# Kernel tuning notes

Hardware: AMD Instinct MI355X
Metric: run time of the kernel (lower is better)

Reference implementation:

```python
import jax, jax.numpy as jnp
import numpy as np
import math

D = 1024
H = 16
FF = 4096
BS = 4
N = 1024
NEG_INF = -jnp.inf


def layer_norm(x, g, b, eps=1e-5):
    mu = jnp.mean(x, axis=-1, keepdims=True)
    var = jnp.var(x, axis=-1, keepdims=True)
    return (x - mu) * jax.lax.rsqrt(var + eps) * g + b


def mha(x, kv, Wq, Wk, Wv, g, b, causal):
    bs, n, d = x.shape
    n_kv = kv.shape[1]
    hd = d // H
    q = (x @ Wq).reshape(bs, n, H, hd)
    k = (kv @ Wk).reshape(bs, n_kv, H, hd)
    v = (kv @ Wv).reshape(bs, n_kv, H, hd)
    # scores scaled by 1/sqrt(model_dim) as in the original (not head_dim!)
    scores = jnp.einsum('bihd,bjhd->bhij', q, k) / math.sqrt(d)
    if causal:
        i = jnp.arange(n)[:, None]
        j = jnp.arange(n_kv)[None, :]
        scores = jnp.where(j <= i, scores, NEG_INF)
    probs = jax.nn.softmax(scores, axis=-1)
    ctx = jnp.einsum('bhij,bjhd->bihd', probs, v).reshape(bs, n, d)
    return layer_norm(ctx + x, g, b)


def setup_inputs() -> dict:
    key = jax.random.key(0)
    ks = jax.random.split(key, 20)
    s_attn = 1.0 / math.sqrt(D)
    s_ff1 = 1.0 / math.sqrt(D)
    s_ff2 = 1.0 / math.sqrt(FF)
    return {
        'x': jax.random.normal(ks[0], (BS, N, D), jnp.float32),
        'encoder_out': jax.random.normal(ks[1], (BS, N, D), jnp.float32),
        'Wq1': jax.random.normal(ks[2], (D, D), jnp.float32) * s_attn,
        'Wk1': jax.random.normal(ks[3], (D, D), jnp.float32) * s_attn,
        'Wv1': jax.random.normal(ks[4], (D, D), jnp.float32) * s_attn,
        'g1': jnp.ones((D,), jnp.float32), 'b1': jnp.zeros((D,), jnp.float32),
        'Wq2': jax.random.normal(ks[5], (D, D), jnp.float32) * s_attn,
        'Wk2': jax.random.normal(ks[6], (D, D), jnp.float32) * s_attn,
        'Wv2': jax.random.normal(ks[7], (D, D), jnp.float32) * s_attn,
        'g2': jnp.ones((D,), jnp.float32), 'b2': jnp.zeros((D,), jnp.float32),
        'W_ff1': jax.random.normal(ks[8], (D, FF), jnp.float32) * s_ff1,
        'b_ff1': jnp.zeros((FF,), jnp.float32),
        'W_ff2': jax.random.normal(ks[9], (FF, D), jnp.float32) * s_ff2,
        'b_ff2': jnp.zeros((D,), jnp.float32),
        'g3': jnp.ones((D,), jnp.float32), 'b3': jnp.zeros((D,), jnp.float32),
    }


def reference(x, encoder_out, Wq1, Wk1, Wv1, g1, b1, Wq2, Wk2, Wv2, g2, b2,
              W_ff1, b_ff1, W_ff2, b_ff2, g3, b3):
    # masked (causal) self-attention
    x = mha(x, x, Wq1, Wk1, Wv1, g1, b1, causal=True)
    # cross-attention over encoder output
    x = mha(x, encoder_out, Wq2, Wk2, Wv2, g2, b2, causal=False)
    # feedforward with exact GELU, residual, layernorm
    h = jax.nn.gelu(x @ W_ff1 + b_ff1, approximate=False)
    out = h @ W_ff2 + b_ff2
    return layer_norm(out + x, g3, b3)
```

## Files before the change

### kernel.cpp

```cpp
#include <hip/hip_runtime.h>

typedef unsigned short u16;
typedef short bf16x8 __attribute__((ext_vector_type(8)));
typedef float f32x4 __attribute__((ext_vector_type(4)));
typedef unsigned short u16x8 __attribute__((ext_vector_type(8)));
typedef unsigned short u16x4 __attribute__((ext_vector_type(4)));

__device__ __forceinline__ u16 f2bf(float f) {
  unsigned u = __builtin_bit_cast(unsigned, f);
  u += 0x7fffu + ((u >> 16) & 1u);
  return (u16)(u >> 16);
}
__device__ __forceinline__ float bf2f(u16 v) {
  return __builtin_bit_cast(float, (unsigned)v << 16);
}

__device__ __forceinline__ void gload_lds16(const void* g, void* l) {
  __builtin_amdgcn_global_load_lds(
      (const __attribute__((address_space(1))) unsigned int*)g,
      (__attribute__((address_space(3))) unsigned int*)l, 16, 0, 0);
}

__global__ __launch_bounds__(256) void cast2_bf16_kernel(const float* __restrict__ s0,
                                                         u16* __restrict__ d0,
                                                         const float* __restrict__ s1,
                                                         u16* __restrict__ d1) {
  const float* s = blockIdx.y ? s1 : s0;
  u16* d = blockIdx.y ? d1 : d0;
  const size_t i = (size_t)blockIdx.x * 256 + threadIdx.x;
  const float4 a = ((const float4*)s)[2 * i];
  const float4 b = ((const float4*)s)[2 * i + 1];
  u16x8 o;
  o[0] = f2bf(a.x); o[1] = f2bf(a.y); o[2] = f2bf(a.z); o[3] = f2bf(a.w);
  o[4] = f2bf(b.x); o[5] = f2bf(b.y); o[6] = f2bf(b.z); o[7] = f2bf(b.w);
  ((u16x8*)d)[i] = o;
}

__global__ __launch_bounds__(256) void pack_mega_kernel(
    const float* __restrict__ W0, const float* __restrict__ W1,
    const float* __restrict__ W2, const float* __restrict__ W3,
    const float* __restrict__ W4, const float* __restrict__ W5,
    const float* __restrict__ W6, const float* __restrict__ W7,
    u16* __restrict__ out) {
  const int bid = blockIdx.x;
  const float* W;
  int K, N, local;
  size_t dst0;
  if (bid < 1536) {
    const int w = bid >> 8;
    local = bid & 255;
    K = 1024; N = 1024;
    W = (w == 0) ? W0 : (w == 1) ? W1 : (w == 2) ? W2 : (w == 3) ? W3 : (w == 4) ? W4 : W5;
    dst0 = (size_t)w * 1024 * 1024;
  } else if (bid < 2560) {
    local = bid - 1536;
    K = 1024; N = 4096; W = W6;
    dst0 = (size_t)6 * 1024 * 1024;
  } else {
    local = bid - 2560;
    K = 4096; N = 1024; W = W7;
    dst0 = (size_t)10 * 1024 * 1024;
  }
  const int nx = N >> 6;
  const int n0 = (local % nx) << 6, k0 = (local / nx) << 6;
  __shared__ u16 sh[64][72];
  const int t = threadIdx.x;
  {
    const int kloc = t >> 2, nc = (t & 3) * 16;
    const float* src = W + (size_t)(k0 + kloc) * N + n0 + nc;
#pragma unroll
    for (int i = 0; i < 16; ++i) sh[kloc][nc + i] = f2bf(src[i]);
  }
  __syncthreads();
  {
    const int nloc = t >> 2, kc = (t & 3) * 16;
    u16 tmp[16];
#pragma unroll
    for (int i = 0; i < 16; ++i) tmp[i] = sh[kc + i][nloc];
    u16* dst = out + dst0 + (size_t)(n0 + nloc) * K + k0 + kc;
    *(u16x8*)dst = *(const u16x8*)tmp;
    *(u16x8*)(dst + 8) = *(const u16x8*)(tmp + 8);
  }
}

template <int EPI, int VOUT>
__global__ __launch_bounds__(512, 4) void gemm_bt(const u16* __restrict__ A,
                                                  const u16* __restrict__ Bt,
                                                  void* __restrict__ Cout,
                                                  const float* __restrict__ bias,
                                                  u16* __restrict__ vt, int voff,
                                                  int M, int N, int K, int lda, int ldb) {
  __shared__ u16 lds[2][2][128 * 64];
  const int tid = threadIdx.x;
  const int lane = tid & 63;
  const int wid = tid >> 6;
  const int wr = wid >> 2;
  const int wc = wid & 3;
  const int g = lane >> 4, cc = lane & 15;
  const int nb = N >> 7;
  const int nwg = gridDim.x;
  const int cpx = nwg >> 3;
  const int bid = (blockIdx.x & 7) * cpx + (blockIdx.x >> 3);
  const int bm = bid / nb, bn = bid % nb;
  const size_t arow0 = (size_t)bm << 7;
  const size_t brow0 = (size_t)bn << 7;
  const size_t koff = (size_t)blockIdx.y * K;

  const u16* ap[2];
  const u16* bp[2];
  int ldst[2];
#pragma unroll
  for (int i = 0; i < 2; ++i) {
    const int tt = i * 512 + tid;
    const int row = tt >> 3;
    const int sc8 = ((tt & 7) ^ (row & 7)) * 8;
    ap[i] = A + (arow0 + row) * lda + koff + sc8;
    bp[i] = Bt + (brow0 + row) * ldb + koff + sc8;
    ldst[i] = (i * 512 + wid * 64) * 8;
  }

  int aoff[4], boff[2];
#pragma unroll
  for (int m = 0; m < 4; ++m) {
    const int rowa = wr * 64 + m * 16 + cc;
    aoff[m] = rowa * 128 + ((g ^ (rowa & 7)) << 4);
  }
#pragma unroll
  for (int n = 0; n < 2; ++n) {
    const int rowb = wc * 32 + n * 16 + cc;
    boff[n] = rowb * 128 + ((g ^ (rowb & 7)) << 4);
  }

  f32x4 acc[4][2] = {};
  const int nk = K >> 6;

#pragma unroll
  for (int i = 0; i < 2; ++i) {
    gload_lds16(ap[i], &lds[0][0][ldst[i]]);
    gload_lds16(bp[i], &lds[0][1][ldst[i]]);
    ap[i] += 64;
    bp[i] += 64;
  }
  __syncthreads();

  int cur = 0;
  for (int kk = 0; kk < nk; ++kk) {
    if (kk + 1 < nk) {
#pragma unroll
      for (int i = 0; i < 2; ++i) {
        gload_lds16(ap[i], &lds[cur ^ 1][0][ldst[i]]);
        gload_lds16(bp[i], &lds[cur ^ 1][1][ldst[i]]);
        ap[i] += 64;
        bp[i] += 64;
      }
    }
    const char* Al = (const char*)&lds[cur][0][0];
    const char* Bl = (const char*)&lds[cur][1][0];
    __builtin_amdgcn_s_setprio(1);
#pragma unroll
    for (int ks = 0; ks < 2; ++ks) {
      const int xr = ks << 6;
      bf16x8 af[4], bfr[2];
#pragma unroll
      for (int m = 0; m < 4; ++m)
        af[m] = *(const bf16x8*)(Al + (aoff[m] ^ xr));
#pragma unroll
      for (int n = 0; n < 2; ++n)
        bfr[n] = *(const bf16x8*)(Bl + (boff[n] ^ xr));
#pragma unroll
      for (int m = 0; m < 4; ++m)
#pragma unroll
        for (int n = 0; n < 2; ++n)
          acc[m][n] = __builtin_amdgcn_mfma_f32_16x16x32_bf16(af[m], bfr[n],
                                                              acc[m][n], 0, 0, 0);
    }
    __builtin_amdgcn_s_setprio(0);
    __syncthreads();
    cur ^= 1;
  }

  const size_t pout = (size_t)blockIdx.y * M * N;
#pragma unroll
  for (int m = 0; m < 4; ++m) {
    const size_t gr0 = arow0 + wr * 64 + m * 16 + (g << 2);
#pragma unroll
    for (int n = 0; n < 2; ++n) {
      const size_t gc = brow0 + wc * 32 + n * 16 + cc;
      if (VOUT && (int)gc >= voff) {
        const int col = (int)gc - voff;
        const int hh = col >> 6, dd = col & 63;
        const int bb = (int)(gr0 >> 10), nn = (int)(gr0 & 1023);
        u16x4 ov;
#pragma unroll
        for (int r = 0; r < 4; ++r) ov[r] = f2bf(acc[m][n][r]);
        *(u16x4*)&vt[(((size_t)(bb * 16 + hh) * 64 + dd) << 10) + nn] = ov;
        continue;
      }
      float bv = 0.f;
      if constexpr (EPI == 1) bv = bias[gc];
#pragma unroll
      for (int r = 0; r < 4; ++r) {
        float v = acc[m][n][r] + bv;
        const size_t idx = (gr0 + r) * (size_t)N + gc;
        if constexpr (EPI == 1) {
          const float u2 = 1.5957691216f * (v + 0.044715f * v * v * v);
          const float e = __expf(u2);
          v = v * e / (e + 1.f);
          ((u16*)Cout)[idx] = f2bf(v);
        } else if constexpr (EPI == 0) {
          ((u16*)Cout)[idx] = f2bf(v);
        } else {
          ((u16*)Cout)[pout + idx] = f2bf(v);
        }
      }
    }
  }
}

template <int CAUSAL, int NZ>
__global__ __launch_bounds__(256, 6) void attn_kernel(const u16* __restrict__ Qb,
                                                      const u16* __restrict__ Kb,
                                                      const u16* __restrict__ Vt,
                                                      u16* __restrict__ Opart,
                                                      float* __restrict__ lpart,
                                                      int qstride, int kstride) {
  const int qt = blockIdx.x;
  const int bh = blockIdx.y;
  const int z = (NZ == 2) ? blockIdx.z : 0;
  const int b = bh >> 4, h = bh & 15;
  const int lane = threadIdx.x & 63;
  const int w = threadIdx.x >> 6;
  const int g = lane >> 4, c = lane & 15;
  const int qbase = qt * 64 + w * 16;

  u16* Op = Opart + (size_t)z * 4096 * 1024;
  float* lp = (NZ == 2) ? lpart + (size_t)z * 64 * 1024 + (size_t)bh * 1024 : nullptr;

  int kt0 = z * (16 / NZ), kt1 = kt0 + 16 / NZ;
  if (CAUSAL) kt1 = min(kt1, qt + 1);

  if (NZ == 2 && kt1 <= kt0) {
#pragma unroll
    for (int r = 0; r < 4; ++r) {
      const int qrow = qbase + g * 4 + r;
      u16x4 zz = {0, 0, 0, 0};
      *(u16x4*)&Op[(size_t)(b * 1024 + qrow) * 1024 + h * 64 + c * 4] = zz;
      if (c == 0) lp[qrow] = 0.f;
    }
    return;
  }

  bf16x8 qf0, qf1;
  {
    const int qrow = qbase + c;
    const u16* qp = Qb + (size_t)(b * 1024 + qrow) * qstride + h * 64 + g * 8;
    qf0 = *(const bf16x8*)qp;
    qf1 = *(const bf16x8*)(qp + 32);
  }

  float l_part[4] = {0.f, 0.f, 0.f, 0.f};
  f32x4 oacc[4] = {};

  __shared__ u16 Kl[64 * 64];
  __shared__ u16 Vl[64 * 64];
  __shared__ u16 Pl[4][16 * 72];
  u16* pw = &Pl[w][0];
  const int tid = threadIdx.x;

  for (int kt = kt0; kt < kt1; ++kt) {
    const int kv0 = kt * 64;
    __syncthreads();
#pragma unroll
    for (int i = 0; i < 2; ++i) {
      const int tt = i * 256 + tid;
      const int row = tt >> 3;
      const int sc = (tt & 7) ^ (row & 7);
      gload_lds16(Kb + (size_t)(b * 1024 + kv0 + row) * kstride + h * 64 + sc * 8,
                  &Kl[(size_t)(i * 256 + w * 64) * 8]);
      gload_lds16(Vt + ((size_t)bh * 64 + row) * 1024 + kv0 + sc * 8,
                  &Vl[(size_t)(i * 256 + w * 64) * 8]);
    }
    __syncthreads();

    f32x4 sacc[4] = {};
#pragma unroll
    for (int t = 0; t < 4; ++t) {
      const int row = t * 16 + c;
      const bf16x8 kf0 = *(const bf16x8*)&Kl[row * 64 + (g ^ (row & 7)) * 8];
      const bf16x8 kf1 = *(const bf16x8*)&Kl[row * 64 + ((4 + g) ^ (row & 7)) * 8];
      sacc[t] = __builtin_amdgcn_mfma_f32_16x16x32_bf16(qf0, kf0, sacc[t], 0, 0, 0);
      sacc[t] = __builtin_amdgcn_mfma_f32_16x16x32_bf16(qf1, kf1, sacc[t], 0, 0, 0);
    }
    const int qr0 = qbase + g * 4;
#pragma unroll
    for (int t = 0; t < 4; ++t) {
      const int kvcol = kv0 + t * 16 + c;
      const int col = t * 16 + c;
#pragma unroll
      for (int r = 0; r < 4; ++r) {
        float p = __expf(sacc[t][r] * 0.03125f);
        if (CAUSAL && kvcol > qr0 + r) p = 0.f;
        l_part[r] += p;
        pw[(g * 4 + r) * 72 + col] = f2bf(p);
      }
    }
#pragma unroll
    for (int ks = 0; ks < 2; ++ks) {
      const bf16x8 pa = *(const bf16x8*)&pw[c * 72 + ks * 32 + g * 8];
#pragma unroll
      for (int t2 = 0; t2 < 4; ++t2) {
        const int row = t2 * 16 + c;
        const bf16x8 vb =
            *(const bf16x8*)&Vl[row * 64 + ((ks * 4 + g) ^ (row & 7)) * 8];
        oacc[t2] = __builtin_amdgcn_mfma_f32_16x16x32_bf16(pa, vb, oacc[t2], 0, 0, 0);
      }
    }
  }
#pragma unroll
  for (int xm = 1; xm < 16; xm <<= 1)
#pragma unroll
    for (int r = 0; r < 4; ++r) l_part[r] += __shfl_xor(l_part[r], xm);

  if constexpr (NZ == 2) {
    if (c == 0) {
#pragma unroll
      for (int r = 0; r < 4; ++r) lp[qbase + g * 4 + r] = l_part[r];
    }
#pragma unroll
    for (int t2 = 0; t2 < 4; ++t2) {
      const int d = t2 * 16 + c;
#pragma unroll
      for (int r = 0; r < 4; ++r) {
        const int qrow = qbase + g * 4 + r;
        Op[(size_t)(b * 1024 + qrow) * 1024 + h * 64 + d] = f2bf(oacc[t2][r]);
      }
    }
  } else {
    float rl[4];
#pragma unroll
    for (int r = 0; r < 4; ++r) rl[r] = 1.f / l_part[r];
#pragma unroll
    for (int t2 = 0; t2 < 4; ++t2) {
      const int d = t2 * 16 + c;
#pragma unroll
      for (int r = 0; r < 4; ++r) {
        const int qrow = qbase + g * 4 + r;
        Op[(size_t)(b * 1024 + qrow) * 1024 + h * 64 + d] = f2bf(oacc[t2][r] * rl[r]);
      }
    }
  }
}

template <int MODE, int RES_BF, int OUT_F>
__global__ __launch_bounds__(256) void add_ln_kernel(const void* __restrict__ a,
                                                     const float* __restrict__ lpart,
                                                     const void* __restrict__ res,
                                                     const float* __restrict__ gam,
                                                     const float* __restrict__ bet,
                                                     float* __restrict__ yf,
                                                     u16* __restrict__ ybf,
                                                     const float* __restrict__ bias) {
  const size_t row = blockIdx.x;
  const int t = threadIdx.x;
  float x[4];
  if constexpr (MODE == 1) {
    const u16* Ob = (const u16*)a;
    const u16x4 p0 = ((const u16x4*)(Ob + row * 1024))[t];
    const u16x4 p1 = ((const u16x4*)(Ob + (size_t)4096 * 1024 + row * 1024))[t];
    const int b = (int)(row >> 10), q = (int)(row & 1023);
    const int h = t >> 4;
    const size_t li = (size_t)(b * 16 + h) * 1024 + q;
    const float inv = 1.f / (lpart[li] + lpart[(size_t)64 * 1024 + li]);
#pragma unroll
    for (int i = 0; i < 4; ++i) x[i] = (bf2f(p0[i]) + bf2f(p1[i])) * inv;
  } else if constexpr (MODE == 2) {
    const u16* Ob = (const u16*)a;
    const u16x4 p0 = ((const u16x4*)(Ob + row * 1024))[t];
    const u16x4 p1 = ((const u16x4*)(Ob + (size_t)4096 * 1024 + row * 1024))[t];
    const float4 bv2 = ((const float4*)bias)[t];
    x[0] = bf2f(p0[0]) + bf2f(p1[0]) + bv2.x;
    x[1] = bf2f(p0[1]) + bf2f(p1[1]) + bv2.y;
    x[2] = bf2f(p0[2]) + bf2f(p1[2]) + bv2.z;
    x[3] = bf2f(p0[3]) + bf2f(p1[3]) + bv2.w;
  } else {
    const u16* Ob = (const u16*)a;
    const u16x4 p0 = ((const u16x4*)(Ob + row * 1024))[t];
#pragma unroll
    for (int i = 0; i < 4; ++i) x[i] = bf2f(p0[i]);
  }
  if constexpr (RES_BF) {
    const u16x4 rv = ((const u16x4*)((const u16*)res + row * 1024))[t];
#pragma unroll
    for (int i = 0; i < 4; ++i) x[i] += bf2f(rv[i]);
  } else {
    const float4 rv = ((const float4*)((const float*)res + row * 1024))[t];
    x[0] += rv.x; x[1] += rv.y; x[2] += rv.z; x[3] += rv.w;
  }
  float s = x[0] + x[1] + x[2] + x[3];
  float q2 = x[0] * x[0] + x[1] * x[1] + x[2] * x[2] + x[3] * x[3];
#pragma unroll
  for (int m = 1; m < 64; m <<= 1) { s += __shfl_xor(s, m); q2 += __shfl_xor(q2, m); }
  __shared__ float ss[4], sq[4];
  const int w = t >> 6;
  if ((t & 63) == 0) { ss[w] = s; sq[w] = q2; }
  __syncthreads();
  s = ss[0] + ss[1] + ss[2] + ss[3];
  q2 = sq[0] + sq[1] + sq[2] + sq[3];
  const float mu = s * (1.f / 1024.f);
  const float var = q2 * (1.f / 1024.f) - mu * mu;
  const float rstd = rsqrtf(var + 1e-5f);
  const float4 gv = ((const float4*)gam)[t];
  const float4 bv = ((const float4*)bet)[t];
  float y[4];
  y[0] = (x[0] - mu) * rstd * gv.x + bv.x;
  y[1] = (x[1] - mu) * rstd * gv.y + bv.y;
  y[2] = (x[2] - mu) * rstd * gv.z + bv.z;
  y[3] = (x[3] - mu) * rstd * gv.w + bv.w;
  if constexpr (OUT_F) {
    float4 o; o.x = y[0]; o.y = y[1]; o.z = y[2]; o.w = y[3];
    ((float4*)(yf + row * 1024))[t] = o;
  } else {
    u16x4 ob;
    ob[0] = f2bf(y[0]); ob[1] = f2bf(y[1]); ob[2] = f2bf(y[2]); ob[3] = f2bf(y[3]);
    ((u16x4*)(ybf + row * 1024))[t] = ob;
  }
}

extern "C" void kernel_launch(void* const* d_in, const int* in_sizes, int n_in,
                              void* d_out, int out_size, void* d_ws, size_t ws_size,
                              hipStream_t stream) {
  const float* x    = (const float*)d_in[0];
  const float* enc  = (const float*)d_in[1];
  const float* Wq1  = (const float*)d_in[2];
  const float* Wk1  = (const float*)d_in[3];
  const float* Wv1  = (const float*)d_in[4];
  const float* g1   = (const float*)d_in[5];
  const float* b1   = (const float*)d_in[6];
  const float* Wq2  = (const float*)d_in[7];
  const float* Wk2  = (const float*)d_in[8];
  const float* Wv2  = (const float*)d_in[9];
  const float* g2   = (const float*)d_in[10];
  const float* b2   = (const float*)d_in[11];
  const float* Wff1 = (const float*)d_in[12];
  const float* bff1 = (const float*)d_in[13];
  const float* Wff2 = (const float*)d_in[14];
  const float* bff2 = (const float*)d_in[15];
  const float* g3   = (const float*)d_in[16];
  const float* b3   = (const float*)d_in[17];
  float* out = (float*)d_out;

  char* ws = (char*)d_ws;
  const size_t MB = 1024ull * 1024ull;
  const size_t M1 = 1024ull * 1024ull;
  u16*   big   = (u16*)(ws + 8 * MB);
  u16*   vt    = (u16*)(ws + 40 * MB);
  u16*   opart = (u16*)(ws + 48 * MB);
  u16*   wpack = (u16*)(ws + 64 * MB);
  float* lpart = (float*)(ws + 92 * MB);
  u16*   abf   = (u16*)(ws + 96 * MB);
  u16*   ebf   = (u16*)(ws + 104 * MB);
  (void)in_sizes; (void)n_in; (void)out_size; (void)ws_size;

  cast2_bf16_kernel<<<dim3(2048, 2), 256, 0, stream>>>(x, abf, enc, ebf);
  pack_mega_kernel<<<3584, 256, 0, stream>>>(Wq1, Wk1, Wv1, Wq2, Wk2, Wv2,
                                             Wff1, Wff2, wpack);

  gemm_bt<0, 1><<<(4096 / 128) * (3072 / 128), 512, 0, stream>>>(
      abf, wpack, big, nullptr, vt, 2048, 4096, 3072, 1024, 1024, 1024);
  attn_kernel<1, 2><<<dim3(16, 64, 2), 256, 0, stream>>>(big, big + 1024, vt,
                                                         opart, lpart, 3072, 3072);
  add_ln_kernel<1, 0, 0><<<4096, 256, 0, stream>>>(opart, lpart, x, g1, b1,
                                                   nullptr, abf, nullptr);

  u16* q2  = big;
  u16* kv2 = big + (size_t)4096 * 1024;
  gemm_bt<0, 0><<<(4096 / 128) * (1024 / 128), 512, 0, stream>>>(
      abf, wpack + 3 * M1, q2, nullptr, nullptr, 0, 4096, 1024, 1024, 1024, 1024);
  gemm_bt<0, 1><<<(4096 / 128) * (2048 / 128), 512, 0, stream>>>(
      ebf, wpack + 4 * M1, kv2, nullptr, vt, 1024, 4096, 2048, 1024, 1024, 1024);
  attn_kernel<0, 1><<<dim3(16, 64, 1), 256, 0, stream>>>(q2, kv2, vt,
                                                         opart, nullptr, 1024, 2048);
  add_ln_kernel<3, 1, 0><<<4096, 256, 0, stream>>>(opart, nullptr, abf, g2, b2,
                                                   nullptr, abf, nullptr);

  gemm_bt<1, 0><<<(4096 / 128) * (4096 / 128), 512, 0, stream>>>(
      abf, wpack + 6 * M1, big, bff1, nullptr, 0, 4096, 4096, 1024, 1024, 1024);
  gemm_bt<3, 0><<<dim3((4096 / 128) * (1024 / 128), 2), 512, 0, stream>>>(
      big, wpack + 10 * M1, opart, nullptr, nullptr, 0, 4096, 1024, 2048, 4096, 4096);
  add_ln_kernel<2, 1, 1><<<4096, 256, 0, stream>>>(opart, nullptr, abf, g3, b3,
                                                   out, nullptr, bff2);
}
```

Before: 269.3 us.

## Add 256x256-tile 8-wave GEMM with 4-way split-K for large projections

Introduces gemm8p, a 256x256 output tile GEMM in which each of 8 waves computes 128x64 and the K loop is split into four quarter phases. Each phase interleaves global-to-LDS prefetch of the next tile with MFMA on the current one. It replaces gemm_bt for the QKV, cross-attention KV and FF1 GEMMs, and for FF2, which now uses a 4-way split-K whose partials go to vt and a spare workspace region and are summed in add_ln. The larger tiles raise arithmetic intensity, at the cost of lower occupancy, fewer workgroups (a wave-quantisation risk), and extra partial-sum traffic.

```diff
diff --git a/kernel.cpp b/kernel.cpp
--- a/kernel.cpp
+++ b/kernel.cpp
@@ -84,6 +84,150 @@
 }
 
 template <int EPI, int VOUT>
+__global__ __launch_bounds__(512, 2) void gemm8p(const u16* __restrict__ A,
+                                                 const u16* __restrict__ Bt,
+                                                 void* __restrict__ Cout,
+                                                 const float* __restrict__ bias,
+                                                 u16* __restrict__ vt, int voff,
+                                                 u16* __restrict__ p3,
+                                                 int M, int N, int K, int lda, int ldb) {
+  __shared__ u16 lds[2][4][128 * 64];
+  const int tid = threadIdx.x;
+  const int lane = tid & 63, wid = tid >> 6;
+  const int wr = wid >> 2, wc = wid & 3;
+  const int g = lane >> 4, cc = lane & 15;
+  const int nb = N >> 8;
+  const int nwg = gridDim.x, cpx = nwg >> 3;
+  const int bid = (blockIdx.x & 7) * cpx + (blockIdx.x >> 3);
+  const int bm = bid / nb, bn = bid % nb;
+  const size_t arow0 = (size_t)bm << 8, brow0 = (size_t)bn << 8;
+  const size_t koff = (size_t)blockIdx.y * K;
+
+  const u16* sp[4][2];
+  int dstu[2];
+#pragma unroll
+  for (int j = 0; j < 2; ++j) {
+    const int p = j * 512 + tid;
+    const int rowh = p >> 3;
+    const int sch = (p & 7) ^ (rowh & 7);
+    sp[0][j] = A + (arow0 + rowh) * lda + koff + sch * 8;
+    sp[1][j] = A + (arow0 + 128 + rowh) * lda + koff + sch * 8;
+    sp[2][j] = Bt + (brow0 + rowh) * ldb + koff + sch * 8;
+    sp[3][j] = Bt + (brow0 + 128 + rowh) * ldb + koff + sch * 8;
+    dstu[j] = (j * 512 + wid * 64) * 8;
+  }
+
+  int aoff[8], boff[4];
+#pragma unroll
+  for (int m = 0; m < 8; ++m) {
+    const int r = m * 16 + cc;
+    aoff[m] = r * 128 + ((g ^ (r & 7)) << 4);
+  }
+#pragma unroll
+  for (int n = 0; n < 4; ++n) {
+    const int r = (wc & 1) * 64 + n * 16 + cc;
+    boff[n] = r * 128 + ((g ^ (r & 7)) << 4);
+  }
+  const int bunit = 2 + (wc >> 1);
+
+  f32x4 acc[8][4] = {};
+  const int nt = K >> 6;
+
+#pragma unroll
+  for (int u = 0; u < 4; ++u)
+#pragma unroll
+    for (int j = 0; j < 2; ++j) {
+      gload_lds16(sp[u][j], &lds[0][u][dstu[j]]);
+      sp[u][j] += 64;
+    }
+
+  for (int t = 0; t < nt; ++t) {
+    asm volatile("s_waitcnt vmcnt(0)" ::: "memory");
+    __builtin_amdgcn_s_barrier();
+    __builtin_amdgcn_sched_barrier(0);
+    const int d = t & 1;
+    const char* Au = (const char*)&lds[d][wr][0];
+    const char* Bu = (const char*)&lds[d][bunit][0];
+    const bool pf = (t + 1 < nt);
+#pragma unroll
+    for (int q = 0; q < 4; ++q) {
+      const int qm = q >> 1, qn = q & 1;
+      bf16x8 af[4][2], bf[2][2];
+#pragma unroll
+      for (int m = 0; m < 4; ++m)
+#pragma unroll
+        for (int ks = 0; ks < 2; ++ks)
+          af[m][ks] = *(const bf16x8*)(Au + (aoff[qm * 4 + m] ^ (ks << 6)));
+#pragma unroll
+      for (int n = 0; n < 2; ++n)
+#pragma unroll
+        for (int ks = 0; ks < 2; ++ks)
+          bf[n][ks] = *(const bf16x8*)(Bu + (boff[qn * 2 + n] ^ (ks << 6)));
+      if (pf) {
+#pragma unroll
+        for (int j = 0; j < 2; ++j) {
+          gload_lds16(sp[q][j], &lds[d ^ 1][q][dstu[j]]);
+          sp[q][j] += 64;
+        }
+      }
+      __builtin_amdgcn_s_barrier();
+      asm volatile("s_waitcnt lgkmcnt(0)" ::: "memory");
+      __builtin_amdgcn_sched_barrier(0);
+      __builtin_amdgcn_s_setprio(1);
+#pragma unroll
+      for (int m = 0; m < 4; ++m)
+#pragma unroll
+        for (int n = 0; n < 2; ++n)
+#pragma unroll
+          for (int ks = 0; ks < 2; ++ks)
+            acc[qm * 4 + m][qn * 2 + n] = __builtin_amdgcn_mfma_f32_16x16x32_bf16(
+                af[m][ks], bf[n][ks], acc[qm * 4 + m][qn * 2 + n], 0, 0, 0);
+      __builtin_amdgcn_s_setprio(0);
+      __builtin_amdgcn_s_barrier();
+    }
+  }
+
+  u16* pdst = nullptr;
+  if constexpr (EPI == 3)
+    pdst = (blockIdx.y < 3) ? (u16*)Cout + (size_t)blockIdx.y * M * N : p3;
+#pragma unroll
+  for (int m = 0; m < 8; ++m) {
+    const size_t gr0 = arow0 + wr * 128 + m * 16 + (g << 2);
+#pragma unroll
+    for (int n = 0; n < 4; ++n) {
+      const size_t gc = brow0 + wc * 64 + n * 16 + cc;
+      if (VOUT && (int)gc >= voff) {
+        const int col = (int)gc - voff;
+        const int hh = col >> 6, dd = col & 63;
+        const int bb = (int)(gr0 >> 10), nn = (int)(gr0 & 1023);
+        u16x4 ov;
+#pragma unroll
+        for (int r = 0; r < 4; ++r) ov[r] = f2bf(acc[m][n][r]);
+        *(u16x4*)&vt[(((size_t)(bb * 16 + hh) * 64 + dd) << 10) + nn] = ov;
+        continue;
+      }
+      float bv = 0.f;
+      if constexpr (EPI == 1) bv = bias[gc];
+#pragma unroll
+      for (int r = 0; r < 4; ++r) {
+        float v = acc[m][n][r] + bv;
+        const size_t idx = (gr0 + r) * (size_t)N + gc;
+        if constexpr (EPI == 1) {
+          const float u2 = 1.5957691216f * (v + 0.044715f * v * v * v);
+          const float e = __expf(u2);
+          v = v * e / (e + 1.f);
+          ((u16*)Cout)[idx] = f2bf(v);
+        } else if constexpr (EPI == 0) {
+          ((u16*)Cout)[idx] = f2bf(v);
+        } else {
+          pdst[idx] = f2bf(v);
+        }
+      }
+    }
+  }
+}
+
+template <int EPI, int VOUT>
 __global__ __launch_bounds__(512, 4) void gemm_bt(const u16* __restrict__ A,
                                                   const u16* __restrict__ Bt,
                                                   void* __restrict__ Cout,
@@ -179,7 +323,6 @@
     cur ^= 1;
   }
 
-  const size_t pout = (size_t)blockIdx.y * M * N;
 #pragma unroll
   for (int m = 0; m < 4; ++m) {
     const size_t gr0 = arow0 + wr * 64 + m * 16 + (g << 2);
@@ -209,8 +352,6 @@
           ((u16*)Cout)[idx] = f2bf(v);
         } else if constexpr (EPI == 0) {
           ((u16*)Cout)[idx] = f2bf(v);
-        } else {
-          ((u16*)Cout)[pout + idx] = f2bf(v);
         }
       }
     }
@@ -375,13 +516,16 @@
     for (int i = 0; i < 4; ++i) x[i] = (bf2f(p0[i]) + bf2f(p1[i])) * inv;
   } else if constexpr (MODE == 2) {
     const u16* Ob = (const u16*)a;
+    const u16* P3 = (const u16*)lpart;
     const u16x4 p0 = ((const u16x4*)(Ob + row * 1024))[t];
     const u16x4 p1 = ((const u16x4*)(Ob + (size_t)4096 * 1024 + row * 1024))[t];
+    const u16x4 p2 = ((const u16x4*)(Ob + (size_t)8192 * 1024 + row * 1024))[t];
+    const u16x4 p3 = ((const u16x4*)(P3 + row * 1024))[t];
     const float4 bv2 = ((const float4*)bias)[t];
-    x[0] = bf2f(p0[0]) + bf2f(p1[0]) + bv2.x;
-    x[1] = bf2f(p0[1]) + bf2f(p1[1]) + bv2.y;
-    x[2] = bf2f(p0[2]) + bf2f(p1[2]) + bv2.z;
-    x[3] = bf2f(p0[3]) + bf2f(p1[3]) + bv2.w;
+    x[0] = bf2f(p0[0]) + bf2f(p1[0]) + bf2f(p2[0]) + bf2f(p3[0]) + bv2.x;
+    x[1] = bf2f(p0[1]) + bf2f(p1[1]) + bf2f(p2[1]) + bf2f(p3[1]) + bv2.y;
+    x[2] = bf2f(p0[2]) + bf2f(p1[2]) + bf2f(p2[2]) + bf2f(p3[2]) + bv2.z;
+    x[3] = bf2f(p0[3]) + bf2f(p1[3]) + bf2f(p2[3]) + bf2f(p3[3]) + bv2.w;
   } else {
     const u16* Ob = (const u16*)a;
     const u16x4 p0 = ((const u16x4*)(Ob + row * 1024))[t];
@@ -452,6 +596,7 @@
   char* ws = (char*)d_ws;
   const size_t MB = 1024ull * 1024ull;
   const size_t M1 = 1024ull * 1024ull;
+  u16*   pextra = (u16*)(ws + 0 * MB);
   u16*   big   = (u16*)(ws + 8 * MB);
   u16*   vt    = (u16*)(ws + 40 * MB);
   u16*   opart = (u16*)(ws + 48 * MB);
@@ -459,14 +604,15 @@
   float* lpart = (float*)(ws + 92 * MB);
   u16*   abf   = (u16*)(ws + 96 * MB);
   u16*   ebf   = (u16*)(ws + 104 * MB);
+  u16*   ffpart = vt;
   (void)in_sizes; (void)n_in; (void)out_size; (void)ws_size;
 
   cast2_bf16_kernel<<<dim3(2048, 2), 256, 0, stream>>>(x, abf, enc, ebf);
   pack_mega_kernel<<<3584, 256, 0, stream>>>(Wq1, Wk1, Wv1, Wq2, Wk2, Wv2,
                                              Wff1, Wff2, wpack);
 
-  gemm_bt<0, 1><<<(4096 / 128) * (3072 / 128), 512, 0, stream>>>(
-      abf, wpack, big, nullptr, vt, 2048, 4096, 3072, 1024, 1024, 1024);
+  gemm8p<0, 1><<<(4096 / 256) * (3072 / 256), 512, 0, stream>>>(
+      abf, wpack, big, nullptr, vt, 2048, nullptr, 4096, 3072, 1024, 1024, 1024);
   attn_kernel<1, 2><<<dim3(16, 64, 2), 256, 0, stream>>>(big, big + 1024, vt,
                                                          opart, lpart, 3072, 3072);
   add_ln_kernel<1, 0, 0><<<4096, 256, 0, stream>>>(opart, lpart, x, g1, b1,
@@ -476,17 +622,18 @@
   u16* kv2 = big + (size_t)4096 * 1024;
   gemm_bt<0, 0><<<(4096 / 128) * (1024 / 128), 512, 0, stream>>>(
       abf, wpack + 3 * M1, q2, nullptr, nullptr, 0, 4096, 1024, 1024, 1024, 1024);
-  gemm_bt<0, 1><<<(4096 / 128) * (2048 / 128), 512, 0, stream>>>(
-      ebf, wpack + 4 * M1, kv2, nullptr, vt, 1024, 4096, 2048, 1024, 1024, 1024);
+  gemm8p<0, 1><<<(4096 / 256) * (2048 / 256), 512, 0, stream>>>(
+      ebf, wpack + 4 * M1, kv2, nullptr, vt, 1024, nullptr, 4096, 2048, 1024, 1024, 1024);
   attn_kernel<0, 1><<<dim3(16, 64, 1), 256, 0, stream>>>(q2, kv2, vt,
                                                          opart, nullptr, 1024, 2048);
   add_ln_kernel<3, 1, 0><<<4096, 256, 0, stream>>>(opart, nullptr, abf, g2, b2,
                                                    nullptr, abf, nullptr);
 
-  gemm_bt<1, 0><<<(4096 / 128) * (4096 / 128), 512, 0, stream>>>(
-      abf, wpack + 6 * M1, big, bff1, nullptr, 0, 4096, 4096, 1024, 1024, 1024);
-  gemm_bt<3, 0><<<dim3((4096 / 128) * (1024 / 128), 2), 512, 0, stream>>>(
-      big, wpack + 10 * M1, opart, nullptr, nullptr, 0, 4096, 1024, 2048, 4096, 4096);
-  add_ln_kernel<2, 1, 1><<<4096, 256, 0, stream>>>(opart, nullptr, abf, g3, b3,
-                                                   out, nullptr, bff2);
-}
+  gemm8p<1, 0><<<(4096 / 256) * (4096 / 256), 512, 0, stream>>>(
+      abf, wpack + 6 * M1, big, bff1, nullptr, 0, nullptr, 4096, 4096, 1024, 1024, 1024);
+  gemm8p<3, 0><<<dim3((4096 / 256) * (1024 / 256), 4), 512, 0, stream>>>(
+      big, wpack + 10 * M1, ffpart, nullptr, nullptr, 0, pextra,
+      4096, 1024, 1024, 4096, 4096);
+  add_ln_kernel<2, 1, 1><<<4096, 256, 0, stream>>>(ffpart, (const float*)pextra, abf,
+                                                   g3, b3, out, nullptr, bff2);
+}
```

Result: slower. 308.0 us (+14.4%).
